# Kernel tuning notes

Hardware: AMD Instinct MI355X
Metric: run time of the kernel (lower is better)

## Reference

```python
import jax, jax.numpy as jnp
import numpy as np

B, S, D = 2, 2048, 1024
H, DK = 16, 64  # num_heads, key_dim (value_dim defaults to key_dim)


def setup_inputs() -> dict:
    key = jax.random.key(0)
    ks = jax.random.split(key, 11)
    init = lambda k, shape, fan_in: jax.random.uniform(
        k, shape, jnp.float32, -1.0, 1.0) * (1.0 / np.sqrt(fan_in))
    return {
        "query": jax.random.normal(ks[0], (B, S, D), jnp.float32),
        "key": jax.random.normal(ks[1], (B, S, D), jnp.float32),
        "value": jax.random.normal(ks[2], (B, S, D), jnp.float32),
        "Wq": init(ks[3], (D, H, DK), D),
        "bq": jnp.zeros((H, DK), jnp.float32),
        "Wk": init(ks[4], (D, H, DK), D),
        "bk": jnp.zeros((H, DK), jnp.float32),
        "Wv": init(ks[5], (D, H, DK), D),
        "bv": jnp.zeros((H, DK), jnp.float32),
        "Wo": init(ks[6], (H, DK, D), H * DK),
        "bo": jnp.zeros((D,), jnp.float32),
    }


def reference(query, key, value, Wq, bq, Wk, bk, Wv, bv, Wo, bo):
    # QKV projections: abc,cde->abde (EinsumDense with bias on (H, DK))
    q = jnp.einsum("bsd,dhk->bshk", query, Wq) + bq  # [B,S,H,DK]
    k = jnp.einsum("bsd,dhk->bshk", key, Wk) + bk
    v = jnp.einsum("bsd,dhk->bshk", value, Wv) + bv
    # Keras scales the query before the dot product
    q = q * (1.0 / jnp.sqrt(jnp.asarray(DK, q.dtype)))
    # aecd,abcd->acbe : [B,H,Sq,Sk]
    scores = jnp.einsum("bqhk,bshk->bhqs", q, k)
    probs = jax.nn.softmax(scores, axis=-1)
    # acbe,aecd->abcd : [B,Sq,H,DK]
    attn = jnp.einsum("bhqs,bshk->bqhk", probs, v)
    # output projection: abcd,cde->abe
    out = jnp.einsum("bqhk,hkd->bqd", attn, Wo) + bo  # [B,S,D]
    return out
```

## Files before the change

kernel.cpp:

```cpp
#include <hip/hip_runtime.h>
#include <hip/hip_bf16.h>
#include <stdint.h>
#include <stddef.h>


typedef __bf16 bf16;
typedef __attribute__((ext_vector_type(4))) bf16 bf16x4;
typedef __attribute__((ext_vector_type(8))) bf16 bf16x8;
typedef __attribute__((ext_vector_type(4))) float f32x4;
typedef __attribute__((ext_vector_type(16))) float f32x16;
typedef __attribute__((ext_vector_type(2))) unsigned int uint2v;

#define DEVINL static __device__ __forceinline__

DEVINL void gload_lds16(const void* g, void* l) {
  __builtin_amdgcn_global_load_lds(
      (const __attribute__((address_space(1))) void*)g,
      (__attribute__((address_space(3))) void*)l, 16, 0, 0);
}

DEVINL f32x4 mfma16(bf16x8 a, bf16x8 b, f32x4 c) {
  return __builtin_amdgcn_mfma_f32_16x16x32_bf16(a, b, c, 0, 0, 0);
}
DEVINL f32x16 mfma32(bf16x8 a, bf16x8 b, f32x16 c) {
  return __builtin_amdgcn_mfma_f32_32x32x16_bf16(a, b, c, 0, 0, 0);
}
DEVINL unsigned pack2(float lo, float hi) {
  union { bf16 h[2]; unsigned u; } t;
  t.h[0] = (bf16)lo; t.h[1] = (bf16)hi;
  return t.u;
}
DEVINL bf16x8 mk8(unsigned a, unsigned b, unsigned c, unsigned d) {
  union { unsigned u[4]; bf16x8 v; } t;
  t.u[0] = a; t.u[1] = b; t.u[2] = c; t.u[3] = d;
  return t.v;
}

__global__ __launch_bounds__(256) void wt_kernel(
    const float* __restrict__ w0, const float* __restrict__ w1,
    const float* __restrict__ w2, const float* __restrict__ w3,
    bf16* __restrict__ out) {
  __shared__ float tile[64 * 65];
  int t = blockIdx.y;
  const float* w = (t == 0) ? w0 : (t == 1) ? w1 : (t == 2) ? w2 : w3;
  bf16* o = out + (size_t)t * 1024 * 1024;
  int tb = blockIdx.x;
  int k0 = (tb >> 4) * 64, n0 = (tb & 15) * 64;
  int c = threadIdx.x & 63, r0 = threadIdx.x >> 6;
  for (int r = r0; r < 64; r += 4)
    tile[r * 65 + c] = w[(size_t)(k0 + r) * 1024 + n0 + c];
  __syncthreads();
  for (int r = r0; r < 64; r += 4)
    o[(size_t)(n0 + r) * 1024 + k0 + c] = (bf16)tile[c * 65 + r];
}

__global__ __launch_bounds__(256) void gemm_qkv(
    const float* __restrict__ Aq, const float* __restrict__ Ak,
    const float* __restrict__ Av, const bf16* __restrict__ Wt,
    const float* __restrict__ bq, const float* __restrict__ bk,
    const float* __restrict__ bv,
    bf16* __restrict__ outQ, bf16* __restrict__ outK, bf16* __restrict__ Vt) {
  int z = blockIdx.z;
  const float* A   = (z == 0) ? Aq : (z == 1) ? Ak : Av;
  const bf16* Wz   = Wt + (size_t)z * 1024 * 1024;
  const float* bia = (z == 0) ? bq : (z == 1) ? bk : bv;
  float scale      = (z == 0) ? 0.125f : 1.0f;

  __shared__ bf16 As[2][128 * 32];
  __shared__ bf16 Bs[2][128 * 32];

  int m0 = blockIdx.x * 128, n0 = blockIdx.y * 128;
  int tid = threadIdx.x, w = tid >> 6, l = tid & 63;
  int wm = (w >> 1) * 64, wn = (w & 1) * 64;
  int c16 = l & 15, g = l >> 4;
  int rsw = (c16 >> 1) & 3;
  int ar = tid >> 1, akb = (tid & 1) * 16;
  int asw = (ar >> 1) & 3;
  int as0 = (((akb >> 3) + 0) ^ asw) * 8;
  int as1 = (((akb >> 3) + 1) ^ asw) * 8;

  int brow0 = (w * 2 + 0) * 16 + (l >> 2);
  int brow1 = (w * 2 + 1) * 16 + (l >> 2);
  int bk0 = ((l & 3) ^ ((brow0 >> 1) & 3)) * 8;
  int bk1 = ((l & 3) ^ ((brow1 >> 1) & 3)) * 8;

  f32x4 acc[4][4] = {};

#define STAGE_B(buf, kt)                                                     \
  do {                                                                       \
    gload_lds16(Wz + (size_t)(n0 + brow0) * 1024 + (kt) + bk0,               \
                (char*)Bs[buf] + (w * 2 + 0) * 1024 + l * 16);               \
    gload_lds16(Wz + (size_t)(n0 + brow1) * 1024 + (kt) + bk1,               \
                (char*)Bs[buf] + (w * 2 + 1) * 1024 + l * 16);               \
  } while (0)

#define PACK_A(buf)                                                          \
  do {                                                                       \
    bf16x8 h0, h1;                                                           \
    _Pragma("unroll") for (int j = 0; j < 4; ++j) {                          \
      h0[j] = (bf16)f0[j]; h0[4 + j] = (bf16)f1[j];                          \
      h1[j] = (bf16)f2[j]; h1[4 + j] = (bf16)f3[j];                          \
    }                                                                        \
    *(bf16x8*)&As[buf][ar * 32 + as0] = h0;                                  \
    *(bf16x8*)&As[buf][ar * 32 + as1] = h1;                                  \
  } while (0)

  STAGE_B(0, 0);
  {
    const float* ap = A + (size_t)(m0 + ar) * 1024 + akb;
    f32x4 f0 = *(const f32x4*)(ap + 0);
    f32x4 f1 = *(const f32x4*)(ap + 4);
    f32x4 f2 = *(const f32x4*)(ap + 8);
    f32x4 f3 = *(const f32x4*)(ap + 12);
    PACK_A(0);
  }
  __syncthreads();

  int cur = 0;
  for (int kt = 0; kt < 1024; kt += 32) {
    f32x4 f0, f1, f2, f3;
    if (kt < 992) {
      STAGE_B(cur ^ 1, kt + 32);
      const float* ap = A + (size_t)(m0 + ar) * 1024 + kt + 32 + akb;
      f0 = *(const f32x4*)(ap + 0);
      f1 = *(const f32x4*)(ap + 4);
      f2 = *(const f32x4*)(ap + 8);
      f3 = *(const f32x4*)(ap + 12);
    }
    bf16x8 af[4], bfr[4];
#pragma unroll
    for (int mt = 0; mt < 4; ++mt)
      af[mt] = *(const bf16x8*)&As[cur][(wm + mt * 16 + c16) * 32 + ((g ^ rsw) * 8)];
#pragma unroll
    for (int nt = 0; nt < 4; ++nt)
      bfr[nt] = *(const bf16x8*)&Bs[cur][(wn + nt * 16 + c16) * 32 + ((g ^ rsw) * 8)];
#pragma unroll
    for (int mt = 0; mt < 4; ++mt)
#pragma unroll
      for (int nt = 0; nt < 4; ++nt)
        acc[mt][nt] = mfma16(af[mt], bfr[nt], acc[mt][nt]);
    if (kt < 992) PACK_A(cur ^ 1);
    __syncthreads();
    cur ^= 1;
  }
#undef STAGE_B
#undef PACK_A

  if (z < 2) {
    bf16* Cout = (z == 0) ? outQ : outK;
#pragma unroll
    for (int mt = 0; mt < 4; ++mt)
#pragma unroll
      for (int nt = 0; nt < 4; ++nt) {
        int n = n0 + wn + nt * 16 + c16;
        float bb = bia[n];
#pragma unroll
        for (int r = 0; r < 4; ++r) {
          int m = m0 + wm + mt * 16 + g * 4 + r;
          Cout[(size_t)m * 1024 + n] = (bf16)((acc[mt][nt][r] + bb) * scale);
        }
      }
  } else {
#pragma unroll
    for (int mt = 0; mt < 4; ++mt)
#pragma unroll
      for (int nt = 0; nt < 4; ++nt) {
        int n = n0 + wn + nt * 16 + c16;
        float bb = bia[n];
        int m = m0 + wm + mt * 16 + g * 4;
        int b = m >> 11, s = m & 2047;
        bf16x4 v;
#pragma unroll
        for (int r = 0; r < 4; ++r) v[r] = (bf16)(acc[mt][nt][r] + bb);
        *(bf16x4*)&Vt[((size_t)(b * 16 + (n >> 6)) * 64 + (n & 63)) * 2048 + s] = v;
      }
  }
}

__global__ __launch_bounds__(256) void flash_kernel(
    const bf16* __restrict__ Qp, const bf16* __restrict__ Kp,
    const bf16* __restrict__ Vt, bf16* __restrict__ AO) {
  __shared__ __align__(16) bf16 Ks[2][64 * 64];
  __shared__ __align__(16) bf16 Vs[2][64 * 64];

  int orig = blockIdx.x;
  int wg = (orig & 7) * 64 + (orig >> 3);
  int bh = wg >> 4, qb = wg & 15;
  int b = bh >> 4, h = bh & 15;
  int tid = threadIdx.x, w = tid >> 6, l = tid & 63;
  int lo5 = l & 31, g = l >> 5;
  int q0 = qb * 128 + w * 32;

  const bf16* qptr = Qp + (size_t)(b * 2048 + q0 + lo5) * 1024 + h * 64 + g * 8;
  bf16x8 qf0 = *(const bf16x8*)(qptr + 0);
  bf16x8 qf1 = *(const bf16x8*)(qptr + 16);
  bf16x8 qf2 = *(const bf16x8*)(qptr + 32);
  bf16x8 qf3 = *(const bf16x8*)(qptr + 48);

  const bf16* kbase = Kp + (size_t)(b * 2048) * 1024 + h * 64;
  const bf16* vbase = Vt + (size_t)bh * 64 * 2048;

  int u0 = w * 64 + l;
  int u1 = (4 + w) * 64 + l;
  int r0s = u0 >> 3, c0s = (u0 & 7) ^ (r0s & 7);
  int r1s = u1 >> 3, c1s = (u1 & 7) ^ (r1s & 7);

#define STAGE(buf, s0)                                                          \
  do {                                                                          \
    gload_lds16(kbase + (size_t)((s0) + r0s) * 1024 + c0s * 8,                  \
                (bf16*)Ks[buf] + u0 * 8);                                       \
    gload_lds16(kbase + (size_t)((s0) + r1s) * 1024 + c1s * 8,                  \
                (bf16*)Ks[buf] + u1 * 8);                                       \
    gload_lds16(vbase + (size_t)r0s * 2048 + (s0) + c0s * 8,                    \
                (bf16*)Vs[buf] + u0 * 8);                                       \
    gload_lds16(vbase + (size_t)r1s * 2048 + (s0) + c1s * 8,                    \
                (bf16*)Vs[buf] + u1 * 8);                                       \
  } while (0)

#define LDSK(cp, nt, kt) \
  (*(const bf16x8*)&cp[(((nt)*32 + lo5) << 6) + (((((kt)*2 + g)) ^ (lo5 & 7)) << 3)])
#define LDSV(cp, dt, st) \
  (*(const bf16x8*)&cp[(((dt)*32 + lo5) << 6) + (((((st)*2 + g)) ^ (lo5 & 7)) << 3)])

  f32x16 o0 = {}, o1 = {};
  float ps0 = 0.f, ps1 = 0.f, ps2 = 0.f, ps3 = 0.f;

  STAGE(0, 0);
  int cur = 0;
  for (int t = 0; t < 32; ++t) {
    if (t < 31) {
      STAGE(cur ^ 1, (t + 1) * 64);
      asm volatile("s_waitcnt vmcnt(4)" ::: "memory");
    } else {
      asm volatile("s_waitcnt vmcnt(0)" ::: "memory");
    }
    __builtin_amdgcn_s_barrier();
    __builtin_amdgcn_sched_barrier(0);
    const bf16* kc = Ks[cur];
    const bf16* vc = Vs[cur];

    f32x16 sv = {};
    sv = mfma32(LDSK(kc, 0, 0), qf0, sv);
    sv = mfma32(LDSK(kc, 0, 1), qf1, sv);
    sv = mfma32(LDSK(kc, 0, 2), qf2, sv);
    sv = mfma32(LDSK(kc, 0, 3), qf3, sv);
    float p[16];
#pragma unroll
    for (int r = 0; r < 16; ++r) p[r] = __expf(sv[r]);
    ps0 += p[0] + p[4] + p[8] + p[12];
    ps1 += p[1] + p[5] + p[9] + p[13];
    ps2 += p[2] + p[6] + p[10] + p[14];
    ps3 += p[3] + p[7] + p[11] + p[15];
    unsigned pw0 = pack2(p[0], p[1]), pw1 = pack2(p[2], p[3]);
    unsigned pw2 = pack2(p[4], p[5]), pw3 = pack2(p[6], p[7]);
    unsigned pw4 = pack2(p[8], p[9]), pw5 = pack2(p[10], p[11]);
    unsigned pw6 = pack2(p[12], p[13]), pw7 = pack2(p[14], p[15]);
    uint2v a02 = __builtin_amdgcn_permlane32_swap(pw0, pw2, false, false);
    uint2v a13 = __builtin_amdgcn_permlane32_swap(pw1, pw3, false, false);
    uint2v a46 = __builtin_amdgcn_permlane32_swap(pw4, pw6, false, false);
    uint2v a57 = __builtin_amdgcn_permlane32_swap(pw5, pw7, false, false);
    bf16x8 pa0 = mk8(a02.x, a13.x, a02.y, a13.y);
    bf16x8 pa1 = mk8(a46.x, a57.x, a46.y, a57.y);

    f32x16 sw = {};
    sw = mfma32(LDSK(kc, 1, 0), qf0, sw);
    sw = mfma32(LDSK(kc, 1, 1), qf1, sw);
    sw = mfma32(LDSK(kc, 1, 2), qf2, sw);
    sw = mfma32(LDSK(kc, 1, 3), qf3, sw);
#pragma unroll
    for (int r = 0; r < 16; ++r) p[r] = __expf(sw[r]);
    ps0 += p[0] + p[4] + p[8] + p[12];
    ps1 += p[1] + p[5] + p[9] + p[13];
    ps2 += p[2] + p[6] + p[10] + p[14];
    ps3 += p[3] + p[7] + p[11] + p[15];
    pw0 = pack2(p[0], p[1]); pw1 = pack2(p[2], p[3]);
    pw2 = pack2(p[4], p[5]); pw3 = pack2(p[6], p[7]);
    pw4 = pack2(p[8], p[9]); pw5 = pack2(p[10], p[11]);
    pw6 = pack2(p[12], p[13]); pw7 = pack2(p[14], p[15]);
    a02 = __builtin_amdgcn_permlane32_swap(pw0, pw2, false, false);
    a13 = __builtin_amdgcn_permlane32_swap(pw1, pw3, false, false);
    a46 = __builtin_amdgcn_permlane32_swap(pw4, pw6, false, false);
    a57 = __builtin_amdgcn_permlane32_swap(pw5, pw7, false, false);
    bf16x8 pb0 = mk8(a02.x, a13.x, a02.y, a13.y);
    bf16x8 pb1 = mk8(a46.x, a57.x, a46.y, a57.y);

    o0 = mfma32(pa0, LDSV(vc, 0, 0), o0);
    o1 = mfma32(pa0, LDSV(vc, 1, 0), o1);
    o0 = mfma32(pa1, LDSV(vc, 0, 1), o0);
    o1 = mfma32(pa1, LDSV(vc, 1, 1), o1);
    o0 = mfma32(pb0, LDSV(vc, 0, 2), o0);
    o1 = mfma32(pb0, LDSV(vc, 1, 2), o1);
    o0 = mfma32(pb1, LDSV(vc, 0, 3), o0);
    o1 = mfma32(pb1, LDSV(vc, 1, 3), o1);

    __builtin_amdgcn_sched_barrier(0);
    __builtin_amdgcn_s_barrier();
    cur ^= 1;
  }
#undef STAGE
#undef LDSK
#undef LDSV

  float plsum = (ps0 + ps1) + (ps2 + ps3);
  float tot = plsum + __shfl_xor(plsum, 32);

#pragma unroll
  for (int r = 0; r < 16; ++r) {
    int qr = (r & 3) + 8 * (r >> 2) + 4 * g;
    float inv = 1.0f / __shfl(tot, qr);
    bf16* op = AO + (size_t)(b * 2048 + q0 + qr) * 1024 + h * 64 + lo5;
    op[0]  = (bf16)(o0[r] * inv);
    op[32] = (bf16)(o1[r] * inv);
  }
}

__global__ __launch_bounds__(256) void gemm_o(
    const bf16* __restrict__ A, const bf16* __restrict__ Wt3,
    const float* __restrict__ bo, float* __restrict__ C) {
  __shared__ bf16 As[2][128 * 32];
  __shared__ bf16 Bs[2][128 * 32];
  int m0 = blockIdx.x * 128, n0 = blockIdx.y * 128;
  int tid = threadIdx.x, w = tid >> 6, l = tid & 63;
  int wm = (w >> 1) * 64, wn = (w & 1) * 64;
  int c16 = l & 15, g = l >> 4;
  int rsw = (c16 >> 1) & 3;

  int brow0 = (w * 2 + 0) * 16 + (l >> 2);
  int brow1 = (w * 2 + 1) * 16 + (l >> 2);
  int bk0 = ((l & 3) ^ ((brow0 >> 1) & 3)) * 8;
  int bk1 = ((l & 3) ^ ((brow1 >> 1) & 3)) * 8;

  f32x4 acc[4][4] = {};

#define STAGE_O(buf, kt)                                                     \
  do {                                                                       \
    gload_lds16(A + (size_t)(m0 + brow0) * 1024 + (kt) + bk0,                \
                (char*)As[buf] + (w * 2 + 0) * 1024 + l * 16);               \
    gload_lds16(A + (size_t)(m0 + brow1) * 1024 + (kt) + bk1,                \
                (char*)As[buf] + (w * 2 + 1) * 1024 + l * 16);               \
    gload_lds16(Wt3 + (size_t)(n0 + brow0) * 1024 + (kt) + bk0,              \
                (char*)Bs[buf] + (w * 2 + 0) * 1024 + l * 16);               \
    gload_lds16(Wt3 + (size_t)(n0 + brow1) * 1024 + (kt) + bk1,              \
                (char*)Bs[buf] + (w * 2 + 1) * 1024 + l * 16);               \
  } while (0)

  STAGE_O(0, 0);
  __syncthreads();

  int cur = 0;
  for (int kt = 0; kt < 1024; kt += 32) {
    if (kt < 992) STAGE_O(cur ^ 1, kt + 32);
    bf16x8 af[4], bfr[4];
#pragma unroll
    for (int mt = 0; mt < 4; ++mt)
      af[mt] = *(const bf16x8*)&As[cur][(wm + mt * 16 + c16) * 32 + ((g ^ rsw) * 8)];
#pragma unroll
    for (int nt = 0; nt < 4; ++nt)
      bfr[nt] = *(const bf16x8*)&Bs[cur][(wn + nt * 16 + c16) * 32 + ((g ^ rsw) * 8)];
#pragma unroll
    for (int mt = 0; mt < 4; ++mt)
#pragma unroll
      for (int nt = 0; nt < 4; ++nt)
        acc[mt][nt] = mfma16(af[mt], bfr[nt], acc[mt][nt]);
    __syncthreads();
    cur ^= 1;
  }
#undef STAGE_O

#pragma unroll
  for (int mt = 0; mt < 4; ++mt)
#pragma unroll
    for (int nt = 0; nt < 4; ++nt) {
      int n = n0 + wn + nt * 16 + c16;
      float bb = bo[n];
#pragma unroll
      for (int r = 0; r < 4; ++r) {
        int m = m0 + wm + mt * 16 + g * 4 + r;
        C[(size_t)m * 1024 + n] = acc[mt][nt][r] + bb;
      }
    }
}

extern "C" void kernel_launch(void* const* d_in, const int* in_sizes, int n_in,
                              void* d_out, int out_size, void* d_ws, size_t ws_size,
                              hipStream_t stream) {
  const float* query = (const float*)d_in[0];
  const float* key_  = (const float*)d_in[1];
  const float* value = (const float*)d_in[2];
  const float* Wq = (const float*)d_in[3];
  const float* bq = (const float*)d_in[4];
  const float* Wk = (const float*)d_in[5];
  const float* bk = (const float*)d_in[6];
  const float* Wv = (const float*)d_in[7];
  const float* bv = (const float*)d_in[8];
  const float* Wo = (const float*)d_in[9];
  const float* bo = (const float*)d_in[10];
  float* out = (float*)d_out;

  char* ws = (char*)d_ws;
  const size_t MB = 1024 * 1024;
  bf16* Wt = (bf16*)(ws);
  bf16* Qp = (bf16*)(ws + 8 * MB);
  bf16* Kp = (bf16*)(ws + 16 * MB);
  bf16* Vt = (bf16*)(ws + 24 * MB);
  bf16* AO = (bf16*)(ws + 32 * MB);

  dim3 blk(256);
  wt_kernel<<<dim3(256, 4), blk, 0, stream>>>(Wq, Wk, Wv, Wo, Wt);
  gemm_qkv<<<dim3(32, 8, 3), blk, 0, stream>>>(query, key_, value, Wt,
                                               bq, bk, bv, Qp, Kp, Vt);
  flash_kernel<<<dim3(512), blk, 0, stream>>>(Qp, Kp, Vt, AO);
  gemm_o<<<dim3(32, 8), blk, 0, stream>>>(AO, Wt + (size_t)3 * 1024 * 1024, bo, out);
}
```

Baseline: 129.5 us.

## Pre-convert activations to bf16, use exp2 with folded log2e scale, raise MFMA priority

A separate kernel converts query/key/value from fp32 to bf16. The QKV GEMM can then stage both A and B tiles straight into LDS with global_load_lds, with no register round trip to pack A. The query scale now folds in log2(e), so the flash kernel can use the raw v_exp_f32 (exp2) instruction in place of __expf. s_setprio is raised around the MFMA groups to favour matrix issue. The cost is an extra kernel launch plus an extra write and read of the bf16 activations (24 MB), and the workspace layout changes so AO reuses the Abf region.

```diff
diff --git a/kernel.cpp b/kernel.cpp
--- a/kernel.cpp
+++ b/kernel.cpp
@@ -24,6 +24,11 @@
 }
 DEVINL f32x16 mfma32(bf16x8 a, bf16x8 b, f32x16 c) {
   return __builtin_amdgcn_mfma_f32_32x32x16_bf16(a, b, c, 0, 0, 0);
+}
+DEVINL float fexp2(float x) {
+  float r;
+  asm("v_exp_f32 %0, %1" : "=v"(r) : "v"(x));
+  return r;
 }
 DEVINL unsigned pack2(float lo, float hi) {
   union { bf16 h[2]; unsigned u; } t;
@@ -54,17 +59,30 @@
     o[(size_t)(n0 + r) * 1024 + k0 + c] = (bf16)tile[c * 65 + r];
 }
 
+__global__ __launch_bounds__(256) void cvt_kernel(
+    const float* __restrict__ q, const float* __restrict__ k,
+    const float* __restrict__ v, bf16* __restrict__ out) {
+  int z = blockIdx.y;
+  const float* src = (z == 0) ? q : (z == 1) ? k : v;
+  size_t off = ((size_t)blockIdx.x * 256 + threadIdx.x) * 8;
+  f32x4 a = *(const f32x4*)(src + off);
+  f32x4 b = *(const f32x4*)(src + off + 4);
+  bf16x8 h;
+#pragma unroll
+  for (int j = 0; j < 4; ++j) { h[j] = (bf16)a[j]; h[4 + j] = (bf16)b[j]; }
+  *(bf16x8*)(out + (size_t)z * 4194304 + off) = h;
+}
+
 __global__ __launch_bounds__(256) void gemm_qkv(
-    const float* __restrict__ Aq, const float* __restrict__ Ak,
-    const float* __restrict__ Av, const bf16* __restrict__ Wt,
+    const bf16* __restrict__ Abf, const bf16* __restrict__ Wt,
     const float* __restrict__ bq, const float* __restrict__ bk,
     const float* __restrict__ bv,
     bf16* __restrict__ outQ, bf16* __restrict__ outK, bf16* __restrict__ Vt) {
   int z = blockIdx.z;
-  const float* A   = (z == 0) ? Aq : (z == 1) ? Ak : Av;
+  const bf16* A    = Abf + (size_t)z * 4194304;
   const bf16* Wz   = Wt + (size_t)z * 1024 * 1024;
   const float* bia = (z == 0) ? bq : (z == 1) ? bk : bv;
-  float scale      = (z == 0) ? 0.125f : 1.0f;
+  float scale      = (z == 0) ? 0.18033688011112042f : 1.0f;
 
   __shared__ bf16 As[2][128 * 32];
   __shared__ bf16 Bs[2][128 * 32];
@@ -74,10 +92,6 @@
   int wm = (w >> 1) * 64, wn = (w & 1) * 64;
   int c16 = l & 15, g = l >> 4;
   int rsw = (c16 >> 1) & 3;
-  int ar = tid >> 1, akb = (tid & 1) * 16;
-  int asw = (ar >> 1) & 3;
-  int as0 = (((akb >> 3) + 0) ^ asw) * 8;
-  int as1 = (((akb >> 3) + 1) ^ asw) * 8;
 
   int brow0 = (w * 2 + 0) * 16 + (l >> 2);
   int brow1 = (w * 2 + 1) * 16 + (l >> 2);
@@ -86,47 +100,24 @@
 
   f32x4 acc[4][4] = {};
 
-#define STAGE_B(buf, kt)                                                     \
+#define STAGE_QKV(buf, kt)                                                   \
   do {                                                                       \
+    gload_lds16(A + (size_t)(m0 + brow0) * 1024 + (kt) + bk0,                \
+                (char*)As[buf] + (w * 2 + 0) * 1024 + l * 16);               \
+    gload_lds16(A + (size_t)(m0 + brow1) * 1024 + (kt) + bk1,                \
+                (char*)As[buf] + (w * 2 + 1) * 1024 + l * 16);               \
     gload_lds16(Wz + (size_t)(n0 + brow0) * 1024 + (kt) + bk0,               \
                 (char*)Bs[buf] + (w * 2 + 0) * 1024 + l * 16);               \
     gload_lds16(Wz + (size_t)(n0 + brow1) * 1024 + (kt) + bk1,               \
                 (char*)Bs[buf] + (w * 2 + 1) * 1024 + l * 16);               \
   } while (0)
 
-#define PACK_A(buf)                                                          \
-  do {                                                                       \
-    bf16x8 h0, h1;                                                           \
-    _Pragma("unroll") for (int j = 0; j < 4; ++j) {                          \
-      h0[j] = (bf16)f0[j]; h0[4 + j] = (bf16)f1[j];                          \
-      h1[j] = (bf16)f2[j]; h1[4 + j] = (bf16)f3[j];                          \
-    }                                                                        \
-    *(bf16x8*)&As[buf][ar * 32 + as0] = h0;                                  \
-    *(bf16x8*)&As[buf][ar * 32 + as1] = h1;                                  \
-  } while (0)
-
-  STAGE_B(0, 0);
-  {
-    const float* ap = A + (size_t)(m0 + ar) * 1024 + akb;
-    f32x4 f0 = *(const f32x4*)(ap + 0);
-    f32x4 f1 = *(const f32x4*)(ap + 4);
-    f32x4 f2 = *(const f32x4*)(ap + 8);
-    f32x4 f3 = *(const f32x4*)(ap + 12);
-    PACK_A(0);
-  }
+  STAGE_QKV(0, 0);
   __syncthreads();
 
   int cur = 0;
   for (int kt = 0; kt < 1024; kt += 32) {
-    f32x4 f0, f1, f2, f3;
-    if (kt < 992) {
-      STAGE_B(cur ^ 1, kt + 32);
-      const float* ap = A + (size_t)(m0 + ar) * 1024 + kt + 32 + akb;
-      f0 = *(const f32x4*)(ap + 0);
-      f1 = *(const f32x4*)(ap + 4);
-      f2 = *(const f32x4*)(ap + 8);
-      f3 = *(const f32x4*)(ap + 12);
-    }
+    if (kt < 992) STAGE_QKV(cur ^ 1, kt + 32);
     bf16x8 af[4], bfr[4];
 #pragma unroll
     for (int mt = 0; mt < 4; ++mt)
@@ -139,12 +130,10 @@
 #pragma unroll
       for (int nt = 0; nt < 4; ++nt)
         acc[mt][nt] = mfma16(af[mt], bfr[nt], acc[mt][nt]);
-    if (kt < 992) PACK_A(cur ^ 1);
     __syncthreads();
     cur ^= 1;
   }
-#undef STAGE_B
-#undef PACK_A
+#undef STAGE_QKV
 
   if (z < 2) {
     bf16* Cout = (z == 0) ? outQ : outK;
@@ -240,13 +229,15 @@
     const bf16* vc = Vs[cur];
 
     f32x16 sv = {};
+    __builtin_amdgcn_s_setprio(1);
     sv = mfma32(LDSK(kc, 0, 0), qf0, sv);
     sv = mfma32(LDSK(kc, 0, 1), qf1, sv);
     sv = mfma32(LDSK(kc, 0, 2), qf2, sv);
     sv = mfma32(LDSK(kc, 0, 3), qf3, sv);
+    __builtin_amdgcn_s_setprio(0);
     float p[16];
 #pragma unroll
-    for (int r = 0; r < 16; ++r) p[r] = __expf(sv[r]);
+    for (int r = 0; r < 16; ++r) p[r] = fexp2(sv[r]);
     ps0 += p[0] + p[4] + p[8] + p[12];
     ps1 += p[1] + p[5] + p[9] + p[13];
     ps2 += p[2] + p[6] + p[10] + p[14];
@@ -263,12 +254,14 @@
     bf16x8 pa1 = mk8(a46.x, a57.x, a46.y, a57.y);
 
     f32x16 sw = {};
+    __builtin_amdgcn_s_setprio(1);
     sw = mfma32(LDSK(kc, 1, 0), qf0, sw);
     sw = mfma32(LDSK(kc, 1, 1), qf1, sw);
     sw = mfma32(LDSK(kc, 1, 2), qf2, sw);
     sw = mfma32(LDSK(kc, 1, 3), qf3, sw);
-#pragma unroll
-    for (int r = 0; r < 16; ++r) p[r] = __expf(sw[r]);
+    __builtin_amdgcn_s_setprio(0);
+#pragma unroll
+    for (int r = 0; r < 16; ++r) p[r] = fexp2(sw[r]);
     ps0 += p[0] + p[4] + p[8] + p[12];
     ps1 += p[1] + p[5] + p[9] + p[13];
     ps2 += p[2] + p[6] + p[10] + p[14];
@@ -284,6 +277,7 @@
     bf16x8 pb0 = mk8(a02.x, a13.x, a02.y, a13.y);
     bf16x8 pb1 = mk8(a46.x, a57.x, a46.y, a57.y);
 
+    __builtin_amdgcn_s_setprio(1);
     o0 = mfma32(pa0, LDSV(vc, 0, 0), o0);
     o1 = mfma32(pa0, LDSV(vc, 1, 0), o1);
     o0 = mfma32(pa1, LDSV(vc, 0, 1), o0);
@@ -292,6 +286,7 @@
     o1 = mfma32(pb0, LDSV(vc, 1, 2), o1);
     o0 = mfma32(pb1, LDSV(vc, 0, 3), o0);
     o1 = mfma32(pb1, LDSV(vc, 1, 3), o1);
+    __builtin_amdgcn_s_setprio(0);
 
     __builtin_amdgcn_sched_barrier(0);
     __builtin_amdgcn_s_barrier();
@@ -399,16 +394,17 @@
 
   char* ws = (char*)d_ws;
   const size_t MB = 1024 * 1024;
-  bf16* Wt = (bf16*)(ws);
-  bf16* Qp = (bf16*)(ws + 8 * MB);
-  bf16* Kp = (bf16*)(ws + 16 * MB);
-  bf16* Vt = (bf16*)(ws + 24 * MB);
-  bf16* AO = (bf16*)(ws + 32 * MB);
+  bf16* Wt  = (bf16*)(ws);
+  bf16* Abf = (bf16*)(ws + 8 * MB);
+  bf16* Qp  = (bf16*)(ws + 32 * MB);
+  bf16* Kp  = (bf16*)(ws + 40 * MB);
+  bf16* Vt  = (bf16*)(ws + 48 * MB);
+  bf16* AO  = (bf16*)(ws + 8 * MB);
 
   dim3 blk(256);
   wt_kernel<<<dim3(256, 4), blk, 0, stream>>>(Wq, Wk, Wv, Wo, Wt);
-  gemm_qkv<<<dim3(32, 8, 3), blk, 0, stream>>>(query, key_, value, Wt,
-                                               bq, bk, bv, Qp, Kp, Vt);
+  cvt_kernel<<<dim3(2048, 3), blk, 0, stream>>>(query, key_, value, Abf);
+  gemm_qkv<<<dim3(32, 8, 3), blk, 0, stream>>>(Abf, Wt, bq, bk, bv, Qp, Kp, Vt);
   flash_kernel<<<dim3(512), blk, 0, stream>>>(Qp, Kp, Vt, AO);
   gemm_o<<<dim3(32, 8), blk, 0, stream>>>(AO, Wt + (size_t)3 * 1024 * 1024, bo, out);
 }
```

Measured after the change: 132.1 us. About the same (+2.0%).
